# Optimization experiments

Hardware: AMD Instinct MI355X
Metric: run time of the kernel (lower is better)

Reference implementation:

```python
import jax, jax.numpy as jnp
import numpy as np
from jax import lax

# dims: batch, in_channels, hidden_size, posenc dim (mid_channels[1]), nF (seq len), proj_size
B, IN_CH, H, FDIM, NF, P = 64, 16, 256, 128, 1001, 1
NL = 3


def _make_f():
    # sinusoidal positional encoding buffer, exactly as in the torch module
    pos = jnp.arange(NF, dtype=jnp.float32).reshape(-1, 1)
    div = jnp.power(jnp.float32(NF), jnp.arange(0, FDIM, 2, dtype=jnp.float32) / FDIM)
    X = pos / div                      # [NF, FDIM//2]
    f = jnp.zeros((NF, FDIM), jnp.float32)
    f = f.at[:, 0::2].set(jnp.sin(X))
    f = f.at[:, 1::2].set(jnp.cos(X))
    return f


def setup_inputs() -> dict:
    key = jax.random.key(0)
    ks = jax.random.split(key, 1 + 5 * NL)
    s = 1.0 / np.sqrt(H)  # torch nn.LSTM init: U(-1/sqrt(H), 1/sqrt(H)); we use scaled normal
    ins = [IN_CH + FDIM, P, P]  # layer input sizes (layers 1,2 receive the projected h, dim P)
    d = {
        "x": jax.random.normal(ks[0], (B, IN_CH), jnp.float32),
        "f": _make_f(),
    }
    for l in range(NL):
        k0, k1, k2, k3, k4 = jax.random.split(ks[1 + l], 5)
        d[f"W_ih{l}"] = jax.random.normal(k0, (4 * H, ins[l]), jnp.float32) * s
        d[f"W_hh{l}"] = jax.random.normal(k1, (4 * H, P), jnp.float32) * s
        d[f"b_ih{l}"] = jax.random.normal(k2, (4 * H,), jnp.float32) * s
        d[f"b_hh{l}"] = jax.random.normal(k3, (4 * H,), jnp.float32) * s
        d[f"W_hr{l}"] = jax.random.normal(k4, (P, H), jnp.float32) * s
    return d


def _lstm_layer(seq, W_ih, W_hh, b_ih, b_hh, W_hr):
    # projected LSTM layer (torch semantics, gate order i, f, g, o)
    Bn, T, _ = seq.shape
    gx = jnp.einsum('bti,gi->btg', seq, W_ih) + (b_ih + b_hh)  # [B, T, 4H]
    h0 = jnp.zeros((Bn, P), seq.dtype)
    c0 = jnp.zeros((Bn, H), seq.dtype)

    def step(carry, gt):
        h, c = carry
        gates = gt + h @ W_hh.T
        i, fg, g, o = jnp.split(gates, 4, axis=-1)
        c = jax.nn.sigmoid(fg) * c + jax.nn.sigmoid(i) * jnp.tanh(g)
        hr = jax.nn.sigmoid(o) * jnp.tanh(c)
        h = hr @ W_hr.T  # projection, no bias
        return (h, c), h

    _, hs = lax.scan(step, (h0, c0), jnp.swapaxes(gx, 0, 1))
    return jnp.swapaxes(hs, 0, 1)  # [B, T, P]


def reference(x, f, W_ih0, W_hh0, b_ih0, b_hh0, W_hr0,
              W_ih1, W_hh1, b_ih1, b_hh1, W_hr1,
              W_ih2, W_hh2, b_ih2, b_hh2, W_hr2):
    Bn = x.shape[0]
    xr = jnp.broadcast_to(x[:, None, :], (Bn, NF, IN_CH))
    fr = jnp.broadcast_to(f[None, :, :], (Bn, NF, FDIM))
    seq = jnp.concatenate([fr, xr], axis=-1)  # [B, NF, FDIM + IN_CH]
    params = [(W_ih0, W_hh0, b_ih0, b_hh0, W_hr0),
              (W_ih1, W_hh1, b_ih1, b_hh1, W_hr1),
              (W_ih2, W_hh2, b_ih2, b_hh2, W_hr2)]
    out = seq
    for p in params:
        out = _lstm_layer(out, *p)
    return out[..., 0]  # squeeze proj dim -> [B, NF]
```

## Files before the change

kernel.cpp:

```cpp
#include <hip/hip_runtime.h>

#define B_DIM 64
#define IN_CH 16
#define H_DIM 256
#define FDIM  128
#define NF    1001
#define INS0  144
#define TB    7
#define U     7
#define NEPOCH 143

#define SC_IFO (-1.44269504088896340736f)
#define SC_G   (-2.88539008177792681472f)

__device__ __forceinline__ float gate_scale(int j) {
    return (j >= 512 && j < 768) ? SC_G : SC_IFO;
}

template<int CTRL, int ROW_MASK>
__device__ __forceinline__ float dpp_add(float x) {
    int y = __builtin_amdgcn_update_dpp(0, __float_as_int(x), CTRL, ROW_MASK, 0xf, true);
    return x + __int_as_float(y);
}
__device__ __forceinline__ float wave_allreduce(float x) {
    x = dpp_add<0x111, 0xf>(x);
    x = dpp_add<0x112, 0xf>(x);
    x = dpp_add<0x114, 0xf>(x);
    x = dpp_add<0x118, 0xf>(x);
    x = dpp_add<0x142, 0xa>(x);
    x = dpp_add<0x143, 0xc>(x);
    return __int_as_float(__builtin_amdgcn_readlane(__float_as_int(x), 63));
}

__global__ __launch_bounds__(1024) void gf_kernel(
    const float* __restrict__ f, const float* __restrict__ W,
    float* __restrict__ Gf)
{
    __shared__ float fs[TB][FDIM];
    const int t0 = blockIdx.x * TB;
    const int tid = threadIdx.x;
    for (int i = tid; i < TB * FDIM; i += 1024)
        fs[i >> 7][i & 127] = f[t0 * FDIM + i];
    __syncthreads();

    const int j = tid;
    const float4* w4 = (const float4*)(W + j * INS0);
    float acc[TB];
#pragma unroll
    for (int t = 0; t < TB; ++t) acc[t] = 0.f;
#pragma unroll
    for (int kc = 0; kc < 8; ++kc) {
        float4 a = w4[kc * 4 + 0];
        float4 b = w4[kc * 4 + 1];
        float4 c = w4[kc * 4 + 2];
        float4 d = w4[kc * 4 + 3];
#pragma unroll
        for (int t = 0; t < TB; ++t) {
            const float* fp = &fs[t][kc * 16];
            float s = acc[t];
            s = fmaf(a.x, fp[0], s);  s = fmaf(a.y, fp[1], s);
            s = fmaf(a.z, fp[2], s);  s = fmaf(a.w, fp[3], s);
            s = fmaf(b.x, fp[4], s);  s = fmaf(b.y, fp[5], s);
            s = fmaf(b.z, fp[6], s);  s = fmaf(b.w, fp[7], s);
            s = fmaf(c.x, fp[8], s);  s = fmaf(c.y, fp[9], s);
            s = fmaf(c.z, fp[10], s); s = fmaf(c.w, fp[11], s);
            s = fmaf(d.x, fp[12], s); s = fmaf(d.y, fp[13], s);
            s = fmaf(d.z, fp[14], s); s = fmaf(d.w, fp[15], s);
            acc[t] = s;
        }
    }
    const float sc = gate_scale(j);
#pragma unroll
    for (int t = 0; t < TB; ++t)
        Gf[(size_t)(t0 + t) * 1024 + j] = acc[t] * sc;
}

__global__ __launch_bounds__(1024) void gxb_kernel(
    const float* __restrict__ x, const float* __restrict__ W,
    const float* __restrict__ bih, const float* __restrict__ bhh,
    float* __restrict__ Gxb)
{
    const int b = blockIdx.x;
    const int j = threadIdx.x;
    const float* w = W + j * INS0 + FDIM;
    const float* xb = x + b * IN_CH;
    float s = bih[j] + bhh[j];
#pragma unroll
    for (int k = 0; k < IN_CH; ++k) s = fmaf(xb[k], w[k], s);
    Gxb[b * 1024 + j] = s * gate_scale(j);
}

__global__ __launch_bounds__(192) void lstm_pipeline(
    const float* __restrict__ Gf, const float* __restrict__ Gxb,
    const float* __restrict__ Whh0, const float* __restrict__ Whr0,
    const float* __restrict__ Wih1, const float* __restrict__ Whh1,
    const float* __restrict__ bih1, const float* __restrict__ bhh1,
    const float* __restrict__ Whr1,
    const float* __restrict__ Wih2, const float* __restrict__ Whh2,
    const float* __restrict__ bih2, const float* __restrict__ bhh2,
    const float* __restrict__ Whr2,
    float* __restrict__ out)
{
    const int b    = blockIdx.x;
    const int wave = threadIdx.x >> 6;
    const int lane = threadIdx.x & 63;
    const int jb   = lane * 4;

    __shared__ float hbuf[3][2][U];

    float base[16];
    float wih[16];
    float whh[16];
    float whr[4];

    const float *whh_p, *whr_p;
    if (wave == 0)      { whh_p = Whh0; whr_p = Whr0; }
    else if (wave == 1) { whh_p = Whh1; whr_p = Whr1; }
    else                { whh_p = Whh2; whr_p = Whr2; }

#pragma unroll
    for (int g = 0; g < 4; ++g) {
        const float sc = (g == 2) ? SC_G : SC_IFO;
        float4 w = *(const float4*)(whh_p + g * 256 + jb);
        whh[g*4+0] = w.x * sc; whh[g*4+1] = w.y * sc;
        whh[g*4+2] = w.z * sc; whh[g*4+3] = w.w * sc;
    }
    {
        float4 w = *(const float4*)(whr_p + jb);
        whr[0] = w.x; whr[1] = w.y; whr[2] = w.z; whr[3] = w.w;
    }

    if (wave == 0) {
#pragma unroll
        for (int g = 0; g < 4; ++g) {
            float4 v = *(const float4*)(Gxb + b * 1024 + g * 256 + jb);
            base[g*4+0] = v.x; base[g*4+1] = v.y; base[g*4+2] = v.z; base[g*4+3] = v.w;
            wih[g*4+0] = 0.f; wih[g*4+1] = 0.f; wih[g*4+2] = 0.f; wih[g*4+3] = 0.f;
        }
    } else {
        const float* bi = (wave == 1) ? bih1 : bih2;
        const float* bh = (wave == 1) ? bhh1 : bhh2;
        const float* wi = (wave == 1) ? Wih1 : Wih2;
#pragma unroll
        for (int g = 0; g < 4; ++g) {
            const float sc = (g == 2) ? SC_G : SC_IFO;
            float4 v1 = *(const float4*)(bi + g * 256 + jb);
            float4 v2 = *(const float4*)(bh + g * 256 + jb);
            float4 v3 = *(const float4*)(wi + g * 256 + jb);
            base[g*4+0] = (v1.x + v2.x) * sc; base[g*4+1] = (v1.y + v2.y) * sc;
            base[g*4+2] = (v1.z + v2.z) * sc; base[g*4+3] = (v1.w + v2.w) * sc;
            wih[g*4+0] = v3.x * sc; wih[g*4+1] = v3.y * sc;
            wih[g*4+2] = v3.z * sc; wih[g*4+3] = v3.w * sc;
        }
    }

    float c4[4] = {0.f, 0.f, 0.f, 0.f};
    float h_state = 0.f;

    for (int e = 0; e < NEPOCH + 2; ++e) {
        __syncthreads();
        const int te = e - wave;
        const bool active = (te >= 0) && (te < NEPOCH);

        float pre[U][16];

        if (active) {
            if (wave == 0) {
                const float* p = Gf + (size_t)te * U * 1024;
#pragma unroll
                for (int u = 0; u < U; ++u) {
#pragma unroll
                    for (int g = 0; g < 4; ++g) {
                        float4 v = *(const float4*)(p + u * 1024 + g * 256 + jb);
                        pre[u][g*4+0] = v.x + base[g*4+0];
                        pre[u][g*4+1] = v.y + base[g*4+1];
                        pre[u][g*4+2] = v.z + base[g*4+2];
                        pre[u][g*4+3] = v.w + base[g*4+3];
                    }
                }
            } else {
                const int par = (e - 1) & 1;
#pragma unroll
                for (int u = 0; u < U; ++u) {
                    float hin = hbuf[wave - 1][par][u];
#pragma unroll
                    for (int i = 0; i < 16; ++i)
                        pre[u][i] = fmaf(hin, wih[i], base[i]);
                }
            }

#pragma unroll
            for (int u = 0; u < U; ++u) {
                float m[4];
#pragma unroll
                for (int jj = 0; jj < 4; ++jj) {
                    float gi_s = fmaf(h_state, whh[0*4+jj], pre[u][0*4+jj]);
                    float gf_s = fmaf(h_state, whh[1*4+jj], pre[u][1*4+jj]);
                    float gg_s = fmaf(h_state, whh[2*4+jj], pre[u][2*4+jj]);
                    float go_s = fmaf(h_state, whh[3*4+jj], pre[u][3*4+jj]);
                    float A  = __builtin_amdgcn_exp2f(gi_s);
                    float Dv = __builtin_amdgcn_exp2f(gf_s);
                    float Bv = __builtin_amdgcn_exp2f(gg_s);
                    float Fv = __builtin_amdgcn_exp2f(go_s);
                    float a1 = 1.f + A, b1 = 1.f + Bv, d1 = 1.f + Dv, f1 = 1.f + Fv;
                    float p1 = a1 * b1;
                    float r1 = __builtin_amdgcn_rcpf(p1 * d1);
                    float si_tg = (1.f - Bv) * d1 * r1;
                    float sf    = p1 * r1;
                    float c  = fmaf(sf, c4[jj], si_tg);
                    c4[jj] = c;
                    float Cv = __builtin_amdgcn_exp2f(SC_G * c);
                    float r2 = __builtin_amdgcn_rcpf(f1 * (1.f + Cv));
                    float hr = (1.f - Cv) * r2;
                    m[jj] = hr * whr[jj];
                }
                float contrib = (m[0] + m[1]) + (m[2] + m[3]);
                float tot = wave_allreduce(contrib);
                h_state = tot;
                if (lane == 0) hbuf[wave][e & 1][u] = tot;
                if (wave == 2 && lane == 0)
                    out[(size_t)b * NF + te * U + u] = tot;
            }
        }
    }
}

extern "C" void kernel_launch(void* const* d_in, const int* in_sizes, int n_in,
                              void* d_out, int out_size, void* d_ws, size_t ws_size,
                              hipStream_t stream)
{
    const float* x    = (const float*)d_in[0];
    const float* f    = (const float*)d_in[1];
    const float* Wih0 = (const float*)d_in[2];
    const float* Whh0 = (const float*)d_in[3];
    const float* bih0 = (const float*)d_in[4];
    const float* bhh0 = (const float*)d_in[5];
    const float* Whr0 = (const float*)d_in[6];
    const float* Wih1 = (const float*)d_in[7];
    const float* Whh1 = (const float*)d_in[8];
    const float* bih1 = (const float*)d_in[9];
    const float* bhh1 = (const float*)d_in[10];
    const float* Whr1 = (const float*)d_in[11];
    const float* Wih2 = (const float*)d_in[12];
    const float* Whh2 = (const float*)d_in[13];
    const float* bih2 = (const float*)d_in[14];
    const float* bhh2 = (const float*)d_in[15];
    const float* Whr2 = (const float*)d_in[16];
    float* out = (float*)d_out;

    float* Gf  = (float*)d_ws;
    float* Gxb = Gf + (size_t)NF * 1024;

    gf_kernel<<<143, 1024, 0, stream>>>(f, Wih0, Gf);
    gxb_kernel<<<64, 1024, 0, stream>>>(x, Wih0, bih0, bhh0, Gxb);
    lstm_pipeline<<<64, 192, 0, stream>>>(Gf, Gxb, Whh0, Whr0,
                                          Wih1, Whh1, bih1, bhh1, Whr1,
                                          Wih2, Whh2, bih2, bhh2, Whr2,
                                          out);
}
```

Measured before the change: 488.0 us.

## Process two batch items per block to interleave independent LSTM recurrences

Each block now carries two batch elements through the three-layer wavefront pipeline, interleaving their independent cell updates and wave reductions. The aim is to hide the serial latency of exp/rcp and DPP all-reduce chains with instruction-level parallelism, and to share Gf loads. Inter-layer hidden values are exchanged as vectorized LDS reads. The trade-off is half as many blocks and higher register pressure per thread.

```diff
diff --git a/kernel.cpp b/kernel.cpp
--- a/kernel.cpp
+++ b/kernel.cpp
@@ -9,6 +9,7 @@
 #define TB    7
 #define U     7
 #define NEPOCH 143
+#define CH    2
 
 #define SC_IFO (-1.44269504088896340736f)
 #define SC_G   (-2.88539008177792681472f)
@@ -30,6 +31,35 @@
     x = dpp_add<0x142, 0xa>(x);
     x = dpp_add<0x143, 0xc>(x);
     return __int_as_float(__builtin_amdgcn_readlane(__float_as_int(x), 63));
+}
+
+__device__ __forceinline__ float lstm_unit4(const float pre[16], const float whh[16],
+                                            const float whr[4], float c4[4], float h)
+{
+    float m[4];
+#pragma unroll
+    for (int jj = 0; jj < 4; ++jj) {
+        float gi_s = fmaf(h, whh[0*4+jj], pre[0*4+jj]);
+        float gf_s = fmaf(h, whh[1*4+jj], pre[1*4+jj]);
+        float gg_s = fmaf(h, whh[2*4+jj], pre[2*4+jj]);
+        float go_s = fmaf(h, whh[3*4+jj], pre[3*4+jj]);
+        float A  = __builtin_amdgcn_exp2f(gi_s);
+        float Dv = __builtin_amdgcn_exp2f(gf_s);
+        float Bv = __builtin_amdgcn_exp2f(gg_s);
+        float Fv = __builtin_amdgcn_exp2f(go_s);
+        float a1 = 1.f + A, b1 = 1.f + Bv, d1 = 1.f + Dv, f1 = 1.f + Fv;
+        float p1 = a1 * b1;
+        float r1 = __builtin_amdgcn_rcpf(p1 * d1);
+        float si_tg = (1.f - Bv) * d1 * r1;
+        float sf    = p1 * r1;
+        float c  = fmaf(sf, c4[jj], si_tg);
+        c4[jj] = c;
+        float Cv = __builtin_amdgcn_exp2f(SC_G * c);
+        float r2 = __builtin_amdgcn_rcpf(f1 * (1.f + Cv));
+        float hr = (1.f - Cv) * r2;
+        m[jj] = hr * whr[jj];
+    }
+    return (m[0] + m[1]) + (m[2] + m[3]);
 }
 
 __global__ __launch_bounds__(1024) void gf_kernel(
@@ -101,14 +131,14 @@
     const float* __restrict__ Whr2,
     float* __restrict__ out)
 {
-    const int b    = blockIdx.x;
+    const int b0   = blockIdx.x * CH;
     const int wave = threadIdx.x >> 6;
     const int lane = threadIdx.x & 63;
     const int jb   = lane * 4;
 
-    __shared__ float hbuf[3][2][U];
-
-    float base[16];
+    __shared__ float hbuf[3][2][CH][8];
+
+    float baseA[16], baseB[16];
     float wih[16];
     float whh[16];
     float whr[4];
@@ -133,8 +163,10 @@
     if (wave == 0) {
 #pragma unroll
         for (int g = 0; g < 4; ++g) {
-            float4 v = *(const float4*)(Gxb + b * 1024 + g * 256 + jb);
-            base[g*4+0] = v.x; base[g*4+1] = v.y; base[g*4+2] = v.z; base[g*4+3] = v.w;
+            float4 va = *(const float4*)(Gxb + (size_t)b0 * 1024 + g * 256 + jb);
+            float4 vb = *(const float4*)(Gxb + (size_t)(b0 + 1) * 1024 + g * 256 + jb);
+            baseA[g*4+0] = va.x; baseA[g*4+1] = va.y; baseA[g*4+2] = va.z; baseA[g*4+3] = va.w;
+            baseB[g*4+0] = vb.x; baseB[g*4+1] = vb.y; baseB[g*4+2] = vb.z; baseB[g*4+3] = vb.w;
             wih[g*4+0] = 0.f; wih[g*4+1] = 0.f; wih[g*4+2] = 0.f; wih[g*4+3] = 0.f;
         }
     } else {
@@ -147,79 +179,72 @@
             float4 v1 = *(const float4*)(bi + g * 256 + jb);
             float4 v2 = *(const float4*)(bh + g * 256 + jb);
             float4 v3 = *(const float4*)(wi + g * 256 + jb);
-            base[g*4+0] = (v1.x + v2.x) * sc; base[g*4+1] = (v1.y + v2.y) * sc;
-            base[g*4+2] = (v1.z + v2.z) * sc; base[g*4+3] = (v1.w + v2.w) * sc;
+            baseA[g*4+0] = (v1.x + v2.x) * sc; baseA[g*4+1] = (v1.y + v2.y) * sc;
+            baseA[g*4+2] = (v1.z + v2.z) * sc; baseA[g*4+3] = (v1.w + v2.w) * sc;
+            baseB[g*4+0] = baseA[g*4+0]; baseB[g*4+1] = baseA[g*4+1];
+            baseB[g*4+2] = baseA[g*4+2]; baseB[g*4+3] = baseA[g*4+3];
             wih[g*4+0] = v3.x * sc; wih[g*4+1] = v3.y * sc;
             wih[g*4+2] = v3.z * sc; wih[g*4+3] = v3.w * sc;
         }
     }
 
-    float c4[4] = {0.f, 0.f, 0.f, 0.f};
-    float h_state = 0.f;
+    float c4A[4] = {0.f, 0.f, 0.f, 0.f};
+    float c4B[4] = {0.f, 0.f, 0.f, 0.f};
+    float hA = 0.f, hB = 0.f;
 
     for (int e = 0; e < NEPOCH + 2; ++e) {
         __syncthreads();
         const int te = e - wave;
-        const bool active = (te >= 0) && (te < NEPOCH);
-
-        float pre[U][16];
-
-        if (active) {
+        if (te < 0 || te >= NEPOCH) continue;
+
+        float hinA[8], hinB[8];
+        if (wave > 0) {
+            const int par = (e - 1) & 1;
+            float4 a0 = *(const float4*)&hbuf[wave - 1][par][0][0];
+            float4 a1 = *(const float4*)&hbuf[wave - 1][par][0][4];
+            float4 b0v = *(const float4*)&hbuf[wave - 1][par][1][0];
+            float4 b1v = *(const float4*)&hbuf[wave - 1][par][1][4];
+            hinA[0]=a0.x; hinA[1]=a0.y; hinA[2]=a0.z; hinA[3]=a0.w;
+            hinA[4]=a1.x; hinA[5]=a1.y; hinA[6]=a1.z; hinA[7]=a1.w;
+            hinB[0]=b0v.x; hinB[1]=b0v.y; hinB[2]=b0v.z; hinB[3]=b0v.w;
+            hinB[4]=b1v.x; hinB[5]=b1v.y; hinB[6]=b1v.z; hinB[7]=b1v.w;
+        }
+
+        const int s_base = te * U;
+#pragma unroll
+        for (int u = 0; u < U; ++u) {
+            float preA[16], preB[16];
             if (wave == 0) {
-                const float* p = Gf + (size_t)te * U * 1024;
-#pragma unroll
-                for (int u = 0; u < U; ++u) {
-#pragma unroll
-                    for (int g = 0; g < 4; ++g) {
-                        float4 v = *(const float4*)(p + u * 1024 + g * 256 + jb);
-                        pre[u][g*4+0] = v.x + base[g*4+0];
-                        pre[u][g*4+1] = v.y + base[g*4+1];
-                        pre[u][g*4+2] = v.z + base[g*4+2];
-                        pre[u][g*4+3] = v.w + base[g*4+3];
-                    }
+                const float* p = Gf + (size_t)(s_base + u) * 1024;
+#pragma unroll
+                for (int g = 0; g < 4; ++g) {
+                    float4 v = *(const float4*)(p + g * 256 + jb);
+                    preA[g*4+0] = v.x + baseA[g*4+0]; preA[g*4+1] = v.y + baseA[g*4+1];
+                    preA[g*4+2] = v.z + baseA[g*4+2]; preA[g*4+3] = v.w + baseA[g*4+3];
+                    preB[g*4+0] = v.x + baseB[g*4+0]; preB[g*4+1] = v.y + baseB[g*4+1];
+                    preB[g*4+2] = v.z + baseB[g*4+2]; preB[g*4+3] = v.w + baseB[g*4+3];
                 }
             } else {
-                const int par = (e - 1) & 1;
-#pragma unroll
-                for (int u = 0; u < U; ++u) {
-                    float hin = hbuf[wave - 1][par][u];
-#pragma unroll
-                    for (int i = 0; i < 16; ++i)
-                        pre[u][i] = fmaf(hin, wih[i], base[i]);
+                const float ha = hinA[u], hb = hinB[u];
+#pragma unroll
+                for (int i = 0; i < 16; ++i) {
+                    preA[i] = fmaf(ha, wih[i], baseA[i]);
+                    preB[i] = fmaf(hb, wih[i], baseB[i]);
                 }
             }
 
-#pragma unroll
-            for (int u = 0; u < U; ++u) {
-                float m[4];
-#pragma unroll
-                for (int jj = 0; jj < 4; ++jj) {
-                    float gi_s = fmaf(h_state, whh[0*4+jj], pre[u][0*4+jj]);
-                    float gf_s = fmaf(h_state, whh[1*4+jj], pre[u][1*4+jj]);
-                    float gg_s = fmaf(h_state, whh[2*4+jj], pre[u][2*4+jj]);
-                    float go_s = fmaf(h_state, whh[3*4+jj], pre[u][3*4+jj]);
-                    float A  = __builtin_amdgcn_exp2f(gi_s);
-                    float Dv = __builtin_amdgcn_exp2f(gf_s);
-                    float Bv = __builtin_amdgcn_exp2f(gg_s);
-                    float Fv = __builtin_amdgcn_exp2f(go_s);
-                    float a1 = 1.f + A, b1 = 1.f + Bv, d1 = 1.f + Dv, f1 = 1.f + Fv;
-                    float p1 = a1 * b1;
-                    float r1 = __builtin_amdgcn_rcpf(p1 * d1);
-                    float si_tg = (1.f - Bv) * d1 * r1;
-                    float sf    = p1 * r1;
-                    float c  = fmaf(sf, c4[jj], si_tg);
-                    c4[jj] = c;
-                    float Cv = __builtin_amdgcn_exp2f(SC_G * c);
-                    float r2 = __builtin_amdgcn_rcpf(f1 * (1.f + Cv));
-                    float hr = (1.f - Cv) * r2;
-                    m[jj] = hr * whr[jj];
-                }
-                float contrib = (m[0] + m[1]) + (m[2] + m[3]);
-                float tot = wave_allreduce(contrib);
-                h_state = tot;
-                if (lane == 0) hbuf[wave][e & 1][u] = tot;
-                if (wave == 2 && lane == 0)
-                    out[(size_t)b * NF + te * U + u] = tot;
+            float contribA = lstm_unit4(preA, whh, whr, c4A, hA);
+            float contribB = lstm_unit4(preB, whh, whr, c4B, hB);
+            float totA = wave_allreduce(contribA);
+            float totB = wave_allreduce(contribB);
+            hA = totA; hB = totB;
+            if (lane == 0) {
+                hbuf[wave][e & 1][0][u] = totA;
+                hbuf[wave][e & 1][1][u] = totB;
+            }
+            if (wave == 2 && lane == 0) {
+                out[(size_t)b0 * NF + s_base + u]       = totA;
+                out[(size_t)(b0 + 1) * NF + s_base + u] = totB;
             }
         }
     }
@@ -253,8 +278,8 @@
 
     gf_kernel<<<143, 1024, 0, stream>>>(f, Wih0, Gf);
     gxb_kernel<<<64, 1024, 0, stream>>>(x, Wih0, bih0, bhh0, Gxb);
-    lstm_pipeline<<<64, 192, 0, stream>>>(Gf, Gxb, Whh0, Whr0,
-                                          Wih1, Whh1, bih1, bhh1, Whr1,
-                                          Wih2, Whh2, bih2, bhh2, Whr2,
-                                          out);
-}
+    lstm_pipeline<<<B_DIM / CH, 192, 0, stream>>>(Gf, Gxb, Whh0, Whr0,
+                                                  Wih1, Whh1, bih1, bhh1, Whr1,
+                                                  Wih2, Whh2, bih2, bhh2, Whr2,
+                                                  out);
+}
```

Result: slower. 942.3 us (+93.1%).

## Split each LSTM layer across four waves with per-timestep wavefront pipelining

Applied to the files above, without the earlier changes.

Changes the recurrent kernel from one wave per layer (each lane holding four hidden units, and layers staggered by a seven-step epoch) to four waves per layer, with one hidden unit per lane. Partial projection sums are exchanged through shared memory, and a block barrier follows every timestep. Layers are now staggered by a single timestep, which shortens the pipeline fill, and layer-0 gate inputs are software-prefetched one epoch ahead. This cuts the per-lane serial work in each step, but it adds a __syncthreads per timestep across 768 threads, which could dominate the latency-bound recurrence.

```diff
diff --git a/kernel.cpp b/kernel.cpp
--- a/kernel.cpp
+++ b/kernel.cpp
@@ -7,8 +7,7 @@
 #define NF    1001
 #define INS0  144
 #define TB    7
-#define U     7
-#define NEPOCH 143
+#define NEP   144
 
 #define SC_IFO (-1.44269504088896340736f)
 #define SC_G   (-2.88539008177792681472f)
@@ -16,20 +15,21 @@
 __device__ __forceinline__ float gate_scale(int j) {
     return (j >= 512 && j < 768) ? SC_G : SC_IFO;
 }
+__device__ __forceinline__ float gsc(int g) { return (g == 2) ? SC_G : SC_IFO; }
 
 template<int CTRL, int ROW_MASK>
 __device__ __forceinline__ float dpp_add(float x) {
     int y = __builtin_amdgcn_update_dpp(0, __float_as_int(x), CTRL, ROW_MASK, 0xf, true);
     return x + __int_as_float(y);
 }
-__device__ __forceinline__ float wave_allreduce(float x) {
+__device__ __forceinline__ float reduce63(float x) {
     x = dpp_add<0x111, 0xf>(x);
     x = dpp_add<0x112, 0xf>(x);
     x = dpp_add<0x114, 0xf>(x);
     x = dpp_add<0x118, 0xf>(x);
     x = dpp_add<0x142, 0xa>(x);
     x = dpp_add<0x143, 0xc>(x);
-    return __int_as_float(__builtin_amdgcn_readlane(__float_as_int(x), 63));
+    return x;
 }
 
 __global__ __launch_bounds__(1024) void gf_kernel(
@@ -90,7 +90,58 @@
     Gxb[b * 1024 + j] = s * gate_scale(j);
 }
 
-__global__ __launch_bounds__(192) void lstm_pipeline(
+__device__ __forceinline__ float4 ldgate(const float* __restrict__ Gf, int t, int j0) {
+    const float* p = Gf + (size_t)t * 1024 + j0;
+    float4 r; r.x = p[0]; r.y = p[256]; r.z = p[512]; r.w = p[768];
+    return r;
+}
+
+__device__ __forceinline__ float step_fn(
+    int k, float4 gv, int lay, int lane, int q,
+    const float whh[4], const float wih[4], const float base[4], float whr0,
+    float& c, float4 (*part4)[2])
+{
+    const int pr = (k - 1) & 1;
+    float4 own = part4[lay][pr];
+    float h = (own.x + own.y) + (own.z + own.w);
+    const bool active = (k >= lay) && (k < NF + lay);
+    if (active) {
+        float pre0, pre1, pre2, pre3;
+        if (lay == 0) {
+            pre0 = gv.x + base[0]; pre1 = gv.y + base[1];
+            pre2 = gv.z + base[2]; pre3 = gv.w + base[3];
+        } else {
+            float4 up = part4[lay - 1][pr];
+            float hin = (up.x + up.y) + (up.z + up.w);
+            pre0 = fmaf(hin, wih[0], base[0]);
+            pre1 = fmaf(hin, wih[1], base[1]);
+            pre2 = fmaf(hin, wih[2], base[2]);
+            pre3 = fmaf(hin, wih[3], base[3]);
+        }
+        float gi = fmaf(h, whh[0], pre0);
+        float gf_ = fmaf(h, whh[1], pre1);
+        float gg = fmaf(h, whh[2], pre2);
+        float go = fmaf(h, whh[3], pre3);
+        float A  = __builtin_amdgcn_exp2f(gi);
+        float Dv = __builtin_amdgcn_exp2f(gf_);
+        float Bv = __builtin_amdgcn_exp2f(gg);
+        float Fv = __builtin_amdgcn_exp2f(go);
+        float a1 = 1.f + A, b1 = 1.f + Bv, d1 = 1.f + Dv, f1 = 1.f + Fv;
+        float p1 = a1 * b1;
+        float r1 = __builtin_amdgcn_rcpf(p1 * d1);
+        float si_tg = (1.f - Bv) * d1 * r1;
+        float sf    = p1 * r1;
+        c = fmaf(sf, c, si_tg);
+        float Cv = __builtin_amdgcn_exp2f(SC_G * c);
+        float r2 = __builtin_amdgcn_rcpf(f1 * (1.f + Cv));
+        float hr = (1.f - Cv) * r2;
+        float m = reduce63(hr * whr0);
+        if (lane == 63) ((float*)&part4[lay][k & 1])[q] = m;
+    }
+    return h;
+}
+
+__global__ __launch_bounds__(768, 3) void lstm_pipeline(
     const float* __restrict__ Gf, const float* __restrict__ Gxb,
     const float* __restrict__ Whh0, const float* __restrict__ Whr0,
     const float* __restrict__ Wih1, const float* __restrict__ Whh1,
@@ -102,125 +153,98 @@
     float* __restrict__ out)
 {
     const int b    = blockIdx.x;
-    const int wave = threadIdx.x >> 6;
+    const int wid  = threadIdx.x >> 6;
     const int lane = threadIdx.x & 63;
-    const int jb   = lane * 4;
-
-    __shared__ float hbuf[3][2][U];
-
-    float base[16];
-    float wih[16];
-    float whh[16];
-    float whr[4];
-
-    const float *whh_p, *whr_p;
-    if (wave == 0)      { whh_p = Whh0; whr_p = Whr0; }
-    else if (wave == 1) { whh_p = Whh1; whr_p = Whr1; }
-    else                { whh_p = Whh2; whr_p = Whr2; }
-
-#pragma unroll
-    for (int g = 0; g < 4; ++g) {
-        const float sc = (g == 2) ? SC_G : SC_IFO;
-        float4 w = *(const float4*)(whh_p + g * 256 + jb);
-        whh[g*4+0] = w.x * sc; whh[g*4+1] = w.y * sc;
-        whh[g*4+2] = w.z * sc; whh[g*4+3] = w.w * sc;
-    }
-    {
-        float4 w = *(const float4*)(whr_p + jb);
-        whr[0] = w.x; whr[1] = w.y; whr[2] = w.z; whr[3] = w.w;
-    }
-
-    if (wave == 0) {
+    const int lay  = wid % 3;
+    const int q    = wid / 3;
+    const int j0   = q * 64 + lane;
+
+    __shared__ float4 part4[3][2];
+    if (threadIdx.x < 24) ((float*)part4)[threadIdx.x] = 0.f;
+
+    const float *whh_p, *whr_p, *wih_p = nullptr, *bi_p = nullptr, *bh_p = nullptr;
+    if (lay == 0)      { whh_p = Whh0; whr_p = Whr0; }
+    else if (lay == 1) { whh_p = Whh1; whr_p = Whr1; wih_p = Wih1; bi_p = bih1; bh_p = bhh1; }
+    else               { whh_p = Whh2; whr_p = Whr2; wih_p = Wih2; bi_p = bih2; bh_p = bhh2; }
+
+    float whh[4], base[4], wih[4];
+#pragma unroll
+    for (int g = 0; g < 4; ++g)
+        whh[g] = whh_p[g * 256 + j0] * gsc(g);
+    const float whr0 = whr_p[j0];
+    if (lay == 0) {
 #pragma unroll
         for (int g = 0; g < 4; ++g) {
-            float4 v = *(const float4*)(Gxb + b * 1024 + g * 256 + jb);
-            base[g*4+0] = v.x; base[g*4+1] = v.y; base[g*4+2] = v.z; base[g*4+3] = v.w;
-            wih[g*4+0] = 0.f; wih[g*4+1] = 0.f; wih[g*4+2] = 0.f; wih[g*4+3] = 0.f;
+            base[g] = Gxb[(size_t)b * 1024 + g * 256 + j0];
+            wih[g] = 0.f;
         }
     } else {
-        const float* bi = (wave == 1) ? bih1 : bih2;
-        const float* bh = (wave == 1) ? bhh1 : bhh2;
-        const float* wi = (wave == 1) ? Wih1 : Wih2;
 #pragma unroll
         for (int g = 0; g < 4; ++g) {
-            const float sc = (g == 2) ? SC_G : SC_IFO;
-            float4 v1 = *(const float4*)(bi + g * 256 + jb);
-            float4 v2 = *(const float4*)(bh + g * 256 + jb);
-            float4 v3 = *(const float4*)(wi + g * 256 + jb);
-            base[g*4+0] = (v1.x + v2.x) * sc; base[g*4+1] = (v1.y + v2.y) * sc;
-            base[g*4+2] = (v1.z + v2.z) * sc; base[g*4+3] = (v1.w + v2.w) * sc;
-            wih[g*4+0] = v3.x * sc; wih[g*4+1] = v3.y * sc;
-            wih[g*4+2] = v3.z * sc; wih[g*4+3] = v3.w * sc;
-        }
-    }
-
-    float c4[4] = {0.f, 0.f, 0.f, 0.f};
-    float h_state = 0.f;
-
-    for (int e = 0; e < NEPOCH + 2; ++e) {
-        __syncthreads();
-        const int te = e - wave;
-        const bool active = (te >= 0) && (te < NEPOCH);
-
-        float pre[U][16];
-
-        if (active) {
-            if (wave == 0) {
-                const float* p = Gf + (size_t)te * U * 1024;
-#pragma unroll
-                for (int u = 0; u < U; ++u) {
-#pragma unroll
-                    for (int g = 0; g < 4; ++g) {
-                        float4 v = *(const float4*)(p + u * 1024 + g * 256 + jb);
-                        pre[u][g*4+0] = v.x + base[g*4+0];
-                        pre[u][g*4+1] = v.y + base[g*4+1];
-                        pre[u][g*4+2] = v.z + base[g*4+2];
-                        pre[u][g*4+3] = v.w + base[g*4+3];
-                    }
-                }
-            } else {
-                const int par = (e - 1) & 1;
-#pragma unroll
-                for (int u = 0; u < U; ++u) {
-                    float hin = hbuf[wave - 1][par][u];
-#pragma unroll
-                    for (int i = 0; i < 16; ++i)
-                        pre[u][i] = fmaf(hin, wih[i], base[i]);
-                }
-            }
-
-#pragma unroll
-            for (int u = 0; u < U; ++u) {
-                float m[4];
-#pragma unroll
-                for (int jj = 0; jj < 4; ++jj) {
-                    float gi_s = fmaf(h_state, whh[0*4+jj], pre[u][0*4+jj]);
-                    float gf_s = fmaf(h_state, whh[1*4+jj], pre[u][1*4+jj]);
-                    float gg_s = fmaf(h_state, whh[2*4+jj], pre[u][2*4+jj]);
-                    float go_s = fmaf(h_state, whh[3*4+jj], pre[u][3*4+jj]);
-                    float A  = __builtin_amdgcn_exp2f(gi_s);
-                    float Dv = __builtin_amdgcn_exp2f(gf_s);
-                    float Bv = __builtin_amdgcn_exp2f(gg_s);
-                    float Fv = __builtin_amdgcn_exp2f(go_s);
-                    float a1 = 1.f + A, b1 = 1.f + Bv, d1 = 1.f + Dv, f1 = 1.f + Fv;
-                    float p1 = a1 * b1;
-                    float r1 = __builtin_amdgcn_rcpf(p1 * d1);
-                    float si_tg = (1.f - Bv) * d1 * r1;
-                    float sf    = p1 * r1;
-                    float c  = fmaf(sf, c4[jj], si_tg);
-                    c4[jj] = c;
-                    float Cv = __builtin_amdgcn_exp2f(SC_G * c);
-                    float r2 = __builtin_amdgcn_rcpf(f1 * (1.f + Cv));
-                    float hr = (1.f - Cv) * r2;
-                    m[jj] = hr * whr[jj];
-                }
-                float contrib = (m[0] + m[1]) + (m[2] + m[3]);
-                float tot = wave_allreduce(contrib);
-                h_state = tot;
-                if (lane == 0) hbuf[wave][e & 1][u] = tot;
-                if (wave == 2 && lane == 0)
-                    out[(size_t)b * NF + te * U + u] = tot;
-            }
+            base[g] = (bi_p[g * 256 + j0] + bh_p[g * 256 + j0]) * gsc(g);
+            wih[g] = wih_p[g * 256 + j0] * gsc(g);
+        }
+    }
+
+    float4 u0{}, u1{}, u2{}, u3{}, u4{}, u5{}, u6{};
+    float4 n0{}, n1{}, n2{}, n3{}, n4{}, n5{}, n6{};
+    if (lay == 0) {
+        n0 = ldgate(Gf, 0, j0); n1 = ldgate(Gf, 1, j0); n2 = ldgate(Gf, 2, j0);
+        n3 = ldgate(Gf, 3, j0); n4 = ldgate(Gf, 4, j0); n5 = ldgate(Gf, 5, j0);
+        n6 = ldgate(Gf, 6, j0);
+    }
+
+    float c = 0.f;
+    float o0 = 0.f, o1 = 0.f, o2 = 0.f, o3 = 0.f, o4 = 0.f, o5 = 0.f, o6 = 0.f;
+    float* outp = out + (size_t)b * NF;
+    const bool isStore = (lay == 2) && (q == 0);
+
+    for (int ep = 0; ep < NEP; ++ep) {
+        const int k0 = ep * 7;
+        float hh;
+
+        __syncthreads();
+        if (lay == 0) {
+            u0 = n0; u1 = n1; u2 = n2; u3 = n3; u4 = n4; u5 = n5; u6 = n6;
+            int tb = k0 + 7;
+            n0 = ldgate(Gf, min(tb + 0, NF - 1), j0);
+            n1 = ldgate(Gf, min(tb + 1, NF - 1), j0);
+            n2 = ldgate(Gf, min(tb + 2, NF - 1), j0);
+            n3 = ldgate(Gf, min(tb + 3, NF - 1), j0);
+            n4 = ldgate(Gf, min(tb + 4, NF - 1), j0);
+            n5 = ldgate(Gf, min(tb + 5, NF - 1), j0);
+            n6 = ldgate(Gf, min(tb + 6, NF - 1), j0);
+        }
+        hh = step_fn(k0 + 0, u0, lay, lane, q, whh, wih, base, whr0, c, part4);
+        if (isStore) o0 = hh;
+        __syncthreads();
+        hh = step_fn(k0 + 1, u1, lay, lane, q, whh, wih, base, whr0, c, part4);
+        if (isStore) o1 = hh;
+        __syncthreads();
+        hh = step_fn(k0 + 2, u2, lay, lane, q, whh, wih, base, whr0, c, part4);
+        if (isStore) o2 = hh;
+        __syncthreads();
+        hh = step_fn(k0 + 3, u3, lay, lane, q, whh, wih, base, whr0, c, part4);
+        if (isStore) o3 = hh;
+        __syncthreads();
+        hh = step_fn(k0 + 4, u4, lay, lane, q, whh, wih, base, whr0, c, part4);
+        if (isStore) o4 = hh;
+        __syncthreads();
+        hh = step_fn(k0 + 5, u5, lay, lane, q, whh, wih, base, whr0, c, part4);
+        if (isStore) o5 = hh;
+        __syncthreads();
+        hh = step_fn(k0 + 6, u6, lay, lane, q, whh, wih, base, whr0, c, part4);
+        if (isStore) o6 = hh;
+
+        if (isStore && lane == 0) {
+            const int tb = k0 - 3;
+            if ((unsigned)(tb + 0) < NF) outp[tb + 0] = o0;
+            if ((unsigned)(tb + 1) < NF) outp[tb + 1] = o1;
+            if ((unsigned)(tb + 2) < NF) outp[tb + 2] = o2;
+            if ((unsigned)(tb + 3) < NF) outp[tb + 3] = o3;
+            if ((unsigned)(tb + 4) < NF) outp[tb + 4] = o4;
+            if ((unsigned)(tb + 5) < NF) outp[tb + 5] = o5;
+            if ((unsigned)(tb + 6) < NF) outp[tb + 6] = o6;
         }
     }
 }
@@ -253,8 +277,8 @@
 
     gf_kernel<<<143, 1024, 0, stream>>>(f, Wih0, Gf);
     gxb_kernel<<<64, 1024, 0, stream>>>(x, Wih0, bih0, bhh0, Gxb);
-    lstm_pipeline<<<64, 192, 0, stream>>>(Gf, Gxb, Whh0, Whr0,
-                                          Wih1, Whh1, bih1, bhh1, Whr1,
-                                          Wih2, Whh2, bih2, bhh2, Whr2,
-                                          out);
-}
+    lstm_pipeline<<<B_DIM, 768, 0, stream>>>(Gf, Gxb, Whh0, Whr0,
+                                             Wih1, Whh1, bih1, bhh1, Whr1,
+                                             Wih2, Whh2, bih2, bhh2, Whr2,
+                                             out);
+}
```

Measured after the change: 544.0 us. 1.11x slower.
